# Kernel tuning notes

Hardware: AMD Instinct MI355X
Metric: run time of the kernel (lower is better)

Reference implementation:

```python
import jax, jax.numpy as jnp
import numpy as np

IN_F = 1024
OUT_F = 1024
R = 16
NUM_USERS = 10000
NUM_ITEMS = 10000
BATCH = 4096
SCALING = 32.0 / 16.0  # lora_alpha / r


def setup_inputs() -> dict:
    key = jax.random.key(0)
    ks = jax.random.split(key, 9)
    return {
        "x": jax.random.normal(ks[0], (BATCH, IN_F), dtype=jnp.float32),
        "user_indices": jax.random.randint(ks[1], (BATCH,), 0, NUM_USERS, dtype=jnp.int32),
        "item_indices": jax.random.randint(ks[2], (BATCH,), 0, NUM_ITEMS, dtype=jnp.int32),
        "W_base": jax.random.normal(ks[3], (OUT_F, IN_F), dtype=jnp.float32) * 0.02,
        "b_base": jax.random.normal(ks[4], (OUT_F,), dtype=jnp.float32) * 0.02,
        "A": jax.random.normal(ks[5], (R, IN_F), dtype=jnp.float32) * 0.02,
        "B_user": jax.random.normal(ks[6], (NUM_USERS, OUT_F, R), dtype=jnp.float32) * 0.02,
        "B_item": jax.random.normal(ks[7], (NUM_ITEMS, OUT_F, R), dtype=jnp.float32) * 0.02,
        "W_common": jax.random.normal(ks[8], (OUT_F, R), dtype=jnp.float32) * 0.02,
    }


def reference(x, user_indices, item_indices, W_base, b_base, A, B_user, B_item, W_common):
    # base linear: [B, out]
    base = x @ W_base.T + b_base
    # lora_A (dropout p=0 -> identity): [B, r]
    a = x @ A.T
    # gather per-row LoRA-B matrices: [B, out, r]
    Bu = B_user[user_indices]
    Bi = B_item[item_indices]
    # batched low-rank matmuls + shared common projection
    user_part = jnp.einsum("bor,br->bo", Bu, a)
    item_part = jnp.einsum("bor,br->bo", Bi, a)
    common_part = a @ W_common.T
    return base + SCALING * (user_part + item_part + common_part)
```

## Files before the change

### kernel.cpp

```cpp
#include <hip/hip_runtime.h>
#include <hip/hip_bf16.h>
#include <cstdint>
#include <cstddef>

typedef __attribute__((ext_vector_type(8))) __bf16 bf16x8;
typedef __attribute__((ext_vector_type(4))) __bf16 bf16x4;
typedef __attribute__((ext_vector_type(4))) float f32x4;

#define BATCH 4096
#define IN_FEAT 1024
#define OUT_FEAT 1024
#define RNK 16
#define SCALE 2.0f

__global__ __launch_bounds__(256) void prep_kernel(
    const float* __restrict__ x, const float* __restrict__ A,
    const float* __restrict__ W, const float* __restrict__ Wc,
    float* __restrict__ a_out, __bf16* __restrict__ x_bf,
    __bf16* __restrict__ w_bf)
{
    __shared__ float xs[IN_FEAT];
    const int b = blockIdx.x;
    const int t = threadIdx.x;
    const int k0 = t * 4;

    if (b < OUT_FEAT) {
        float4 wv = *reinterpret_cast<const float4*>(&W[(size_t)b * IN_FEAT + k0]);
        float cx = 0.f, cy = 0.f, cz = 0.f, cw = 0.f;
        #pragma unroll
        for (int r = 0; r < RNK; ++r) {
            const float wcr = Wc[b * RNK + r];
            const float4 av = *reinterpret_cast<const float4*>(&A[r * IN_FEAT + k0]);
            cx += wcr * av.x; cy += wcr * av.y; cz += wcr * av.z; cw += wcr * av.w;
        }
        bf16x4 hw;
        hw[0] = (__bf16)(wv.x + SCALE * cx);
        hw[1] = (__bf16)(wv.y + SCALE * cy);
        hw[2] = (__bf16)(wv.z + SCALE * cz);
        hw[3] = (__bf16)(wv.w + SCALE * cw);
        *reinterpret_cast<bf16x4*>(&w_bf[(size_t)b * IN_FEAT + k0]) = hw;
    }

    const float4 v = *reinterpret_cast<const float4*>(&x[(size_t)b * IN_FEAT + k0]);
    xs[k0 + 0] = v.x; xs[k0 + 1] = v.y; xs[k0 + 2] = v.z; xs[k0 + 3] = v.w;
    bf16x4 h;
    h[0] = (__bf16)v.x; h[1] = (__bf16)v.y; h[2] = (__bf16)v.z; h[3] = (__bf16)v.w;
    *reinterpret_cast<bf16x4*>(&x_bf[(size_t)b * IN_FEAT + k0]) = h;
    __syncthreads();

    const int r = t >> 4;
    const int l16 = t & 15;
    const float* __restrict__ Ar = &A[r * IN_FEAT];
    float s = 0.f;
    #pragma unroll 8
    for (int j = 0; j < IN_FEAT / 16; ++j) {
        const int k = l16 + 16 * j;
        s += xs[k] * Ar[k];
    }
    s += __shfl_xor(s, 8);
    s += __shfl_xor(s, 4);
    s += __shfl_xor(s, 2);
    s += __shfl_xor(s, 1);
    if (l16 == 0) a_out[b * RNK + r] = s;
}

#define BM 64
#define BN 64
#define BK 64
#define LDK 72

__global__ __launch_bounds__(256) void fused_kernel(
    const __bf16* __restrict__ x_bf, const __bf16* __restrict__ w_bf,
    const float* __restrict__ a_buf,
    const int* __restrict__ uidx, const int* __restrict__ iidx,
    const float* __restrict__ b_base,
    const float* __restrict__ B_user, const float* __restrict__ B_item,
    float* __restrict__ out)
{
    __shared__ __align__(16) __bf16 xs[BM * LDK];
    __shared__ __align__(16) __bf16 wsh[BN * LDK];
    __shared__ __align__(16) float a_s[BM * RNK];
    __shared__ __align__(16) float lora_s[BM * BN];
    __shared__ int u_s[BM];
    __shared__ int i_s[BM];

    const int t = threadIdx.x;

    const int bid = blockIdx.y * gridDim.x + blockIdx.x;
    const int nid = (bid & 7) * 128 + (bid >> 3);
    const int o0 = (nid & 15) * BN;
    const int b0 = (nid >> 4) * BM;

    if (t < BM) {
        u_s[t] = uidx[b0 + t];
        i_s[t] = iidx[b0 + t];
    }
    *reinterpret_cast<float4*>(&a_s[t * 4]) =
        *reinterpret_cast<const float4*>(&a_buf[(size_t)b0 * RNK + t * 4]);

    const int w  = t >> 6;
    const int wr = w >> 1;
    const int wc = w & 1;
    const int l  = t & 63;
    const int lr = l & 15;
    const int lg = l >> 4;

    const int srow  = t >> 2;
    const int skoff = (t & 3) * 16;

    f32x4 acc[2][2] = {};

    #pragma unroll
    for (int kt = 0; kt < IN_FEAT / BK; ++kt) {
        __syncthreads();
        {
            const uint4* g = reinterpret_cast<const uint4*>(
                &x_bf[(size_t)(b0 + srow) * IN_FEAT + kt * BK + skoff]);
            uint4 v0 = g[0], v1 = g[1];
            *reinterpret_cast<uint4*>(&xs[srow * LDK + skoff]) = v0;
            *reinterpret_cast<uint4*>(&xs[srow * LDK + skoff + 8]) = v1;
            const uint4* gw = reinterpret_cast<const uint4*>(
                &w_bf[(size_t)(o0 + srow) * IN_FEAT + kt * BK + skoff]);
            uint4 w0 = gw[0], w1 = gw[1];
            *reinterpret_cast<uint4*>(&wsh[srow * LDK + skoff]) = w0;
            *reinterpret_cast<uint4*>(&wsh[srow * LDK + skoff + 8]) = w1;
        }
        __syncthreads();

        const int bl = w * 16 + kt;
        const size_t u  = (size_t)u_s[bl];
        const size_t iv = (size_t)i_s[bl];
        const f32x4* bu = reinterpret_cast<const f32x4*>(
            &B_user[(u * OUT_FEAT + (size_t)(o0 + l)) * RNK]);
        const f32x4* bi = reinterpret_cast<const f32x4*>(
            &B_item[(iv * OUT_FEAT + (size_t)(o0 + l)) * RNK]);
        f32x4 gu0 = bu[0], gu1 = bu[1], gu2 = bu[2], gu3 = bu[3];
        f32x4 gi0 = bi[0], gi1 = bi[1], gi2 = bi[2], gi3 = bi[3];

        #pragma unroll
        for (int kk = 0; kk < BK; kk += 32) {
            bf16x8 af0 = *reinterpret_cast<const bf16x8*>(&xs[(wr * 32 + 0 + lr) * LDK + kk + lg * 8]);
            bf16x8 af1 = *reinterpret_cast<const bf16x8*>(&xs[(wr * 32 + 16 + lr) * LDK + kk + lg * 8]);
            bf16x8 bf0 = *reinterpret_cast<const bf16x8*>(&wsh[(wc * 32 + 0 + lr) * LDK + kk + lg * 8]);
            bf16x8 bf1 = *reinterpret_cast<const bf16x8*>(&wsh[(wc * 32 + 16 + lr) * LDK + kk + lg * 8]);
            acc[0][0] = __builtin_amdgcn_mfma_f32_16x16x32_bf16(af0, bf0, acc[0][0], 0, 0, 0);
            acc[0][1] = __builtin_amdgcn_mfma_f32_16x16x32_bf16(af0, bf1, acc[0][1], 0, 0, 0);
            acc[1][0] = __builtin_amdgcn_mfma_f32_16x16x32_bf16(af1, bf0, acc[1][0], 0, 0, 0);
            acc[1][1] = __builtin_amdgcn_mfma_f32_16x16x32_bf16(af1, bf1, acc[1][1], 0, 0, 0);
        }

        {
            const f32x4* av4 = reinterpret_cast<const f32x4*>(&a_s[bl * RNK]);
            float lora = 0.f;
            const f32x4 s0 = gu0 + gi0, a0 = av4[0];
            lora += s0[0]*a0[0] + s0[1]*a0[1] + s0[2]*a0[2] + s0[3]*a0[3];
            const f32x4 s1 = gu1 + gi1, a1 = av4[1];
            lora += s1[0]*a1[0] + s1[1]*a1[1] + s1[2]*a1[2] + s1[3]*a1[3];
            const f32x4 s2 = gu2 + gi2, a2 = av4[2];
            lora += s2[0]*a2[0] + s2[1]*a2[1] + s2[2]*a2[2] + s2[3]*a2[3];
            const f32x4 s3 = gu3 + gi3, a3 = av4[3];
            lora += s3[0]*a3[0] + s3[1]*a3[1] + s3[2]*a3[2] + s3[3]*a3[3];
            lora_s[bl * BN + l] = SCALE * lora;
        }
    }

    __syncthreads();

    #pragma unroll
    for (int n = 0; n < 2; ++n) {
        const int ol = wc * 32 + n * 16 + lr;
        const int o  = o0 + ol;
        const float bb = b_base[o];
        #pragma unroll
        for (int m = 0; m < 2; ++m) {
            #pragma unroll
            for (int i = 0; i < 4; ++i) {
                const int bl2 = wr * 32 + m * 16 + lg * 4 + i;
                out[(size_t)(b0 + bl2) * OUT_FEAT + o] =
                    acc[m][n][i] + bb + lora_s[bl2 * BN + ol];
            }
        }
    }
}

extern "C" void kernel_launch(void* const* d_in, const int* in_sizes, int n_in,
                              void* d_out, int out_size, void* d_ws, size_t ws_size,
                              hipStream_t stream) {
    const float* x        = (const float*)d_in[0];
    const int*   uidx     = (const int*)d_in[1];
    const int*   iidx     = (const int*)d_in[2];
    const float* W_base   = (const float*)d_in[3];
    const float* b_base   = (const float*)d_in[4];
    const float* A        = (const float*)d_in[5];
    const float* B_user   = (const float*)d_in[6];
    const float* B_item   = (const float*)d_in[7];
    const float* W_common = (const float*)d_in[8];
    float* out = (float*)d_out;

    float*  a_buf = (float*)d_ws;
    __bf16* x_bf  = (__bf16*)((char*)d_ws + (256 << 10));
    __bf16* w_bf  = (__bf16*)((char*)d_ws + (256 << 10) + (8 << 20));

    prep_kernel<<<BATCH, 256, 0, stream>>>(x, A, W_base, W_common, a_buf, x_bf, w_bf);

    dim3 grid(OUT_FEAT / BN, BATCH / BM);
    fused_kernel<<<grid, 256, 0, stream>>>(x_bf, w_bf, a_buf, uidx, iidx,
                                           b_base, B_user, B_item, out);
}
```

Baseline: 122.2 us.

## Widen fused GEMM tile to 64x128 with 512 threads and padded LoRA buffer

```diff
diff --git a/kernel.cpp b/kernel.cpp
--- a/kernel.cpp
+++ b/kernel.cpp
@@ -65,11 +65,12 @@
 }
 
 #define BM 64
-#define BN 64
+#define BN 128
 #define BK 64
 #define LDK 72
-
-__global__ __launch_bounds__(256) void fused_kernel(
+#define LSTRIDE 132
+
+__global__ __launch_bounds__(512) void fused_kernel(
     const __bf16* __restrict__ x_bf, const __bf16* __restrict__ w_bf,
     const float* __restrict__ a_buf,
     const int* __restrict__ uidx, const int* __restrict__ iidx,
@@ -80,33 +81,37 @@
     __shared__ __align__(16) __bf16 xs[BM * LDK];
     __shared__ __align__(16) __bf16 wsh[BN * LDK];
     __shared__ __align__(16) float a_s[BM * RNK];
-    __shared__ __align__(16) float lora_s[BM * BN];
+    __shared__ __align__(16) float lora_s[BM * LSTRIDE];
     __shared__ int u_s[BM];
     __shared__ int i_s[BM];
 
     const int t = threadIdx.x;
 
     const int bid = blockIdx.y * gridDim.x + blockIdx.x;
-    const int nid = (bid & 7) * 128 + (bid >> 3);
-    const int o0 = (nid & 15) * BN;
-    const int b0 = (nid >> 4) * BM;
+    const int nid = (bid & 7) * 64 + (bid >> 3);
+    const int o0 = (nid & 7) * BN;
+    const int b0 = (nid >> 3) * BM;
 
     if (t < BM) {
         u_s[t] = uidx[b0 + t];
         i_s[t] = iidx[b0 + t];
     }
-    *reinterpret_cast<float4*>(&a_s[t * 4]) =
-        *reinterpret_cast<const float4*>(&a_buf[(size_t)b0 * RNK + t * 4]);
+    if (t < 256) {
+        *reinterpret_cast<float4*>(&a_s[t * 4]) =
+            *reinterpret_cast<const float4*>(&a_buf[(size_t)b0 * RNK + t * 4]);
+    }
 
     const int w  = t >> 6;
-    const int wr = w >> 1;
-    const int wc = w & 1;
+    const int wr = w >> 2;
+    const int wc = w & 3;
     const int l  = t & 63;
     const int lr = l & 15;
     const int lg = l >> 4;
 
-    const int srow  = t >> 2;
-    const int skoff = (t & 3) * 16;
+    const int xrow = t >> 3;
+    const int xoff = (t & 7) * 8;
+    const int wrow = t >> 2;
+    const int woff = (t & 3) * 16;
 
     f32x4 acc[2][2] = {};
 
@@ -115,25 +120,25 @@
         __syncthreads();
         {
             const uint4* g = reinterpret_cast<const uint4*>(
-                &x_bf[(size_t)(b0 + srow) * IN_FEAT + kt * BK + skoff]);
-            uint4 v0 = g[0], v1 = g[1];
-            *reinterpret_cast<uint4*>(&xs[srow * LDK + skoff]) = v0;
-            *reinterpret_cast<uint4*>(&xs[srow * LDK + skoff + 8]) = v1;
+                &x_bf[(size_t)(b0 + xrow) * IN_FEAT + kt * BK + xoff]);
+            uint4 v0 = g[0];
+            *reinterpret_cast<uint4*>(&xs[xrow * LDK + xoff]) = v0;
             const uint4* gw = reinterpret_cast<const uint4*>(
-                &w_bf[(size_t)(o0 + srow) * IN_FEAT + kt * BK + skoff]);
+                &w_bf[(size_t)(o0 + wrow) * IN_FEAT + kt * BK + woff]);
             uint4 w0 = gw[0], w1 = gw[1];
-            *reinterpret_cast<uint4*>(&wsh[srow * LDK + skoff]) = w0;
-            *reinterpret_cast<uint4*>(&wsh[srow * LDK + skoff + 8]) = w1;
+            *reinterpret_cast<uint4*>(&wsh[wrow * LDK + woff]) = w0;
+            *reinterpret_cast<uint4*>(&wsh[wrow * LDK + woff + 8]) = w1;
         }
         __syncthreads();
 
-        const int bl = w * 16 + kt;
-        const size_t u  = (size_t)u_s[bl];
-        const size_t iv = (size_t)i_s[bl];
+        const int grow = w * 8 + (kt >> 1);
+        const int gcol = (kt & 1) * 64 + l;
+        const size_t u  = (size_t)u_s[grow];
+        const size_t iv = (size_t)i_s[grow];
         const f32x4* bu = reinterpret_cast<const f32x4*>(
-            &B_user[(u * OUT_FEAT + (size_t)(o0 + l)) * RNK]);
+            &B_user[(u * OUT_FEAT + (size_t)(o0 + gcol)) * RNK]);
         const f32x4* bi = reinterpret_cast<const f32x4*>(
-            &B_item[(iv * OUT_FEAT + (size_t)(o0 + l)) * RNK]);
+            &B_item[(iv * OUT_FEAT + (size_t)(o0 + gcol)) * RNK]);
         f32x4 gu0 = bu[0], gu1 = bu[1], gu2 = bu[2], gu3 = bu[3];
         f32x4 gi0 = bi[0], gi1 = bi[1], gi2 = bi[2], gi3 = bi[3];
 
@@ -150,7 +155,7 @@
         }
 
         {
-            const f32x4* av4 = reinterpret_cast<const f32x4*>(&a_s[bl * RNK]);
+            const f32x4* av4 = reinterpret_cast<const f32x4*>(&a_s[grow * RNK]);
             float lora = 0.f;
             const f32x4 s0 = gu0 + gi0, a0 = av4[0];
             lora += s0[0]*a0[0] + s0[1]*a0[1] + s0[2]*a0[2] + s0[3]*a0[3];
@@ -160,7 +165,7 @@
             lora += s2[0]*a2[0] + s2[1]*a2[1] + s2[2]*a2[2] + s2[3]*a2[3];
             const f32x4 s3 = gu3 + gi3, a3 = av4[3];
             lora += s3[0]*a3[0] + s3[1]*a3[1] + s3[2]*a3[2] + s3[3]*a3[3];
-            lora_s[bl * BN + l] = SCALE * lora;
+            lora_s[grow * LSTRIDE + gcol] = SCALE * lora;
         }
     }
 
@@ -177,7 +182,7 @@
             for (int i = 0; i < 4; ++i) {
                 const int bl2 = wr * 32 + m * 16 + lg * 4 + i;
                 out[(size_t)(b0 + bl2) * OUT_FEAT + o] =
-                    acc[m][n][i] + bb + lora_s[bl2 * BN + ol];
+                    acc[m][n][i] + bb + lora_s[bl2 * LSTRIDE + ol];
             }
         }
     }
@@ -204,6 +209,6 @@
     prep_kernel<<<BATCH, 256, 0, stream>>>(x, A, W_base, W_common, a_buf, x_bf, w_bf);
 
     dim3 grid(OUT_FEAT / BN, BATCH / BM);
-    fused_kernel<<<grid, 256, 0, stream>>>(x_bf, w_bf, a_buf, uidx, iidx,
+    fused_kernel<<<grid, 512, 0, stream>>>(x_bf, w_bf, a_buf, uidx, iidx,
                                            b_base, B_user, B_item, out);
 }
```

After: 128.6 us. +5.3%, slower.
